# Kernel optimization log

Measured on AMD Instinct MI355X. Metric: run time of the kernel, lower is better.

The kernel has to match this reference:

```python
import jax, jax.numpy as jnp
import numpy as np

M, N, D, P, N_kv = 512, 4096, 128, 3584, 1024
H, H_kv = N // D, N_kv // D          # 32 query heads, 8 kv heads
G = H // H_kv                        # group size 4
L = P + M                            # cache length 4096


def setup_inputs() -> dict:
    key = jax.random.key(0)
    ks = jax.random.split(key, 6)
    w_scale = 0.008  # ~0.5/sqrt(N): keeps unscaled exp-softmax logits in fp32 range
    return {
        "X": jax.random.normal(ks[0], (M, N), jnp.float32),
        "W_q": jax.random.normal(ks[1], (N, N), jnp.float32) * w_scale,
        "W_k": jax.random.normal(ks[2], (N, N_kv), jnp.float32) * w_scale,
        "W_v": jax.random.normal(ks[3], (N, N_kv), jnp.float32) * w_scale,
        "cache_K": jax.random.normal(ks[4], (H, L, D), jnp.float32) * 0.02,
        "cache_V": jax.random.normal(ks[5], (H, L, D), jnp.float32) * 0.02,
    }


def reference(X, W_q, W_k, W_v, cache_K, cache_V):
    # fused QKV projection
    W_qkv = jnp.concatenate([W_q, W_k, W_v], axis=1)        # [N, N + 2*N_kv]
    qkv = X @ W_qkv                                          # [M, N + 2*N_kv]
    q = qkv[:, :N].reshape(M, H, D).transpose(1, 0, 2)       # [H, M, D]
    k = qkv[:, N:N + N_kv].reshape(M, H_kv, D).transpose(1, 0, 2)   # [H_kv, M, D]
    v = qkv[:, N + N_kv:].reshape(M, H_kv, D).transpose(1, 0, 2)    # [H_kv, M, D]
    # expand grouped KV heads (repeat_interleave) and append to cache at P
    k_exp = jnp.repeat(k, G, axis=0)                         # [H, M, D]
    v_exp = jnp.repeat(v, G, axis=0)
    Kc = cache_K.at[:, P:P + M, :].set(k_exp)                # [H, L, D]
    Vc = cache_V.at[:, P:P + M, :].set(v_exp)
    # naive (unscaled, non-max-subtracted) softmax attention over full cache
    scores = jnp.einsum('hmd,hld->hml', q, Kc)               # [H, M, L]
    e = jnp.exp(scores)
    weights = e / jnp.sum(e, axis=-1, keepdims=True)
    out = jnp.einsum('hml,hld->hmd', weights, Vc)            # [H, M, D]
    return out.transpose(1, 0, 2).reshape(M, H * D)          # [M, N]
```

## Files before the change

### kernel.cpp

```cpp
#include <hip/hip_runtime.h>
#include <hip/hip_bf16.h>

typedef __attribute__((ext_vector_type(8))) short short8;
typedef __attribute__((ext_vector_type(4))) float f32x4;

#define M_   512
#define N_   4096
#define D_   128
#define P_   3584
#define NKV  1024
#define L_   4096
#define H_   32
#define LOG2E 1.44269504088896340736f

__device__ __forceinline__ ushort f2bf(float f) {
  union { float f; unsigned u; } v; v.f = f;
  unsigned r = (v.u + 0x7fffu + ((v.u >> 16) & 1u)) >> 16;
  return (ushort)r;
}
__device__ __forceinline__ float bf2f(ushort u) {
  union { unsigned u; float f; } v; v.u = ((unsigned)u) << 16;
  return v.f;
}
__device__ __forceinline__ float fexp2(float x) {
  return __builtin_amdgcn_exp2f(x);
}
__device__ __forceinline__ unsigned pk2bf(float a, float b) {
  union { __hip_bfloat162 h; unsigned u; } cv;
  cv.h = __float22bfloat162_rn(make_float2(a, b));
  return cv.u;
}

__device__ __forceinline__ void gload_lds16(const void* g, void* l) {
  __builtin_amdgcn_global_load_lds(
      (const __attribute__((address_space(1))) void*)g,
      (__attribute__((address_space(3))) void*)l, 16, 0, 0);
}

__global__ __launch_bounds__(256) void xconv(const float* __restrict__ X,
                                             ushort* __restrict__ Xs)
{
  int g = blockIdx.x * 256 + threadIdx.x;
  int row = g >> 9;
  int cir = g & 511;
  int grp = cir >> 3, ch = cir & 7;
  const float* src = &X[(size_t)row * 4096 + cir * 8];
  float4 f0 = *reinterpret_cast<const float4*>(src);
  float4 f1 = *reinterpret_cast<const float4*>(src + 4);
  short8 s;
  s[0] = f2bf(f0.x); s[1] = f2bf(f0.y); s[2] = f2bf(f0.z); s[3] = f2bf(f0.w);
  s[4] = f2bf(f1.x); s[5] = f2bf(f1.y); s[6] = f2bf(f1.z); s[7] = f2bf(f1.w);
  int dcol = grp * 64 + ((ch ^ (row & 7)) * 8);
  *reinterpret_cast<short8*>(&Xs[(size_t)row * 4096 + dcol]) = s;
}

__global__ __launch_bounds__(256) void wtrans(
    const float* __restrict__ Wq, const float* __restrict__ Wk,
    const float* __restrict__ Wv, ushort* __restrict__ Wt)
{
  int bx = blockIdx.x;
  int by = blockIdx.y;
  const float* W; int wcols, c0;
  if (by < 64)      { W = Wq; wcols = 4096; c0 = by * 64; }
  else if (by < 80) { W = Wk; wcols = 1024; c0 = (by - 64) * 64; }
  else              { W = Wv; wcols = 1024; c0 = (by - 80) * 64; }
  int orow0 = by * 64;
  int r0 = bx * 64;
  __shared__ float T[64][65];
  int tid = threadIdx.x;

  #pragma unroll
  for (int i = 0; i < 4; ++i) {
    int r = i * 16 + (tid >> 4);
    int c4 = tid & 15;
    float4 f = *reinterpret_cast<const float4*>(&W[(size_t)(r0 + r) * wcols + c0 + c4 * 4]);
    T[r][c4 * 4 + 0] = f.x; T[r][c4 * 4 + 1] = f.y;
    T[r][c4 * 4 + 2] = f.z; T[r][c4 * 4 + 3] = f.w;
  }
  __syncthreads();

  #pragma unroll
  for (int i = 0; i < 2; ++i) {
    int j = i * 256 + tid;
    int orr = j >> 3;
    int ch = j & 7;
    short8 s;
    #pragma unroll
    for (int e = 0; e < 8; ++e) s[e] = f2bf(T[ch * 8 + e][orr]);
    int orow = orow0 + orr;
    int dstch = ch ^ (orow & 7);
    *reinterpret_cast<short8*>(&Wt[(size_t)orow * 4096 + r0 + dstch * 8]) = s;
  }
}

#define GEMM_STAGE(buf, k0g) do {                                             \
    _Pragma("unroll")                                                         \
    for (int i_ = 0; i_ < 4; ++i_) {                                          \
      int blk_ = w * 4 + i_;                                                  \
      gload_lds16(Asrc + (size_t)(blk_ * 8 + (lane >> 3)) * 4096 + (k0g) + (lane & 7) * 8, \
                  &As[buf][blk_ * 512]);                                      \
    }                                                                         \
    _Pragma("unroll")                                                         \
    for (int i_ = 0; i_ < 4; ++i_) {                                          \
      int blk_ = w * 4 + i_;                                                  \
      gload_lds16(Bsrc + (size_t)(blk_ * 8 + (lane >> 3)) * 4096 + (k0g) + (lane & 7) * 8, \
                  &Bs[buf][blk_ * 512]);                                      \
    }                                                                         \
  } while (0)

__global__ __launch_bounds__(256, 2) void qkv_gemm3(
    const ushort* __restrict__ Xs, const ushort* __restrict__ Wt,
    float* __restrict__ pg)
{
  const int bx = blockIdx.x;
  const int by = blockIdx.y;
  const int bz = blockIdx.z;
  const int tid = threadIdx.x, lane = tid & 63, w = tid >> 6;
  const int wr = w >> 1, wc = w & 1;
  const int m0 = by * 128, n0 = bx * 128;
  const int kb0 = bz * 2048;

  __shared__ ushort As[2][128 * 64];
  __shared__ ushort Bs[2][128 * 64];

  f32x4 acc[4][4];
  #pragma unroll
  for (int m = 0; m < 4; ++m)
    #pragma unroll
    for (int n = 0; n < 4; ++n)
      acc[m][n] = (f32x4){0.f, 0.f, 0.f, 0.f};

  const ushort* Asrc = Xs + (size_t)m0 * 4096;
  const ushort* Bsrc = Wt + (size_t)n0 * 4096;

  GEMM_STAGE(0, kb0);
  __syncthreads();
  int cur = 0;

  for (int kt = 0; kt < 32; ++kt) {
    if (kt + 1 < 32) GEMM_STAGE(cur ^ 1, kb0 + (kt + 1) * 64);
    #pragma unroll
    for (int kk = 0; kk < 2; ++kk) {
      short8 a[4], b[4];
      #pragma unroll
      for (int m = 0; m < 4; ++m) {
        int row = wr * 64 + m * 16 + (lane & 15);
        int ch = (kk * 4 + (lane >> 4)) ^ (row & 7);
        a[m] = *reinterpret_cast<const short8*>(&As[cur][row * 64 + ch * 8]);
      }
      #pragma unroll
      for (int n = 0; n < 4; ++n) {
        int row = wc * 64 + n * 16 + (lane & 15);
        int ch = (kk * 4 + (lane >> 4)) ^ (row & 7);
        b[n] = *reinterpret_cast<const short8*>(&Bs[cur][row * 64 + ch * 8]);
      }
      #pragma unroll
      for (int m = 0; m < 4; ++m)
        #pragma unroll
        for (int n = 0; n < 4; ++n)
          acc[m][n] = __builtin_amdgcn_mfma_f32_16x16x32_bf16(a[m], b[n], acc[m][n], 0, 0, 0);
    }
    __syncthreads();
    cur ^= 1;
  }

  float* dst = pg + (size_t)bz * 512 * 6144;
  #pragma unroll
  for (int m = 0; m < 4; ++m)
    #pragma unroll
    for (int n = 0; n < 4; ++n)
      #pragma unroll
      for (int j = 0; j < 4; ++j) {
        int row = m0 + wr * 64 + m * 16 + (lane >> 4) * 4 + j;
        int col = n0 + wc * 64 + n * 16 + (lane & 15);
        dst[(size_t)row * 6144 + col] = acc[m][n][j];
      }
}

__global__ __launch_bounds__(256) void combine_qk(
    const float* __restrict__ pg, ushort* __restrict__ qb,
    ushort* __restrict__ Kbn)
{
  int id = blockIdx.x * 256 + threadIdx.x;
  int m = id / 640;
  int c8 = (id - m * 640) * 8;
  const float* p0 = pg + (size_t)m * 6144 + c8;
  const float* p1 = p0 + (size_t)512 * 6144;
  if (c8 < 4096) {
    short8 s;
    #pragma unroll
    for (int e = 0; e < 8; ++e) s[e] = f2bf((p0[e] + p1[e]) * LOG2E);
    *reinterpret_cast<short8*>(&qb[(size_t)m * 4096 + c8]) = s;
  } else {
    short8 s;
    #pragma unroll
    for (int e = 0; e < 8; ++e) s[e] = f2bf(p0[e] + p1[e]);
    int o = c8 - 4096;
    int hk = o >> 7, d0 = o & 127;
    #pragma unroll
    for (int g = 0; g < 4; ++g)
      *reinterpret_cast<short8*>(&Kbn[((size_t)(hk * 4 + g) * 512 + m) * 128 + d0]) = s;
  }
}

__global__ __launch_bounds__(256) void combine_v(
    const float* __restrict__ pg, ushort* __restrict__ Vtn)
{
  int bz = blockIdx.x;
  int mt = bz & 7, hk = (bz >> 3) & 7, dh = bz >> 6;
  int m0 = mt * 64;
  int d0 = dh * 64;
  int colbase = 5120 + hk * 128 + d0;
  __shared__ float T[64][65];
  int tid = threadIdx.x;
  int r = tid >> 2, q4 = tid & 3;

  #pragma unroll
  for (int i = 0; i < 4; ++i) {
    int c = (q4 * 4 + i) * 4;
    const float* p0 = pg + (size_t)(m0 + r) * 6144 + colbase + c;
    const float* p1 = p0 + (size_t)512 * 6144;
    float4 a = *reinterpret_cast<const float4*>(p0);
    float4 b = *reinterpret_cast<const float4*>(p1);
    T[r][c + 0] = a.x + b.x; T[r][c + 1] = a.y + b.y;
    T[r][c + 2] = a.z + b.z; T[r][c + 3] = a.w + b.w;
  }
  __syncthreads();

  #pragma unroll
  for (int p = 0; p < 2; ++p) {
    int idx = p * 256 + tid;
    int dloc = idx >> 3, cc = idx & 7;
    int half = cc >> 2, c4 = (cc & 3) * 4;
    short8 s;
    #pragma unroll
    for (int e = 0; e < 8; ++e) {
      int lrow = half * 32 + c4 + (e < 4 ? e : 16 + (e - 4));
      s[e] = f2bf(T[lrow][dloc]);
    }
    int d = d0 + dloc;
    #pragma unroll
    for (int g = 0; g < 4; ++g) {
      int h = hk * 4 + g;
      *reinterpret_cast<short8*>(&Vtn[((size_t)h * 128 + d) * (size_t)L_ + P_ + m0 + cc * 8]) = s;
    }
  }
}

__global__ __launch_bounds__(256) void vconv(
    const float* __restrict__ cacheV, ushort* __restrict__ Vtn)
{
  int h = blockIdx.x, lt = blockIdx.y, dh = blockIdx.z;
  int l0 = lt * 64, d0 = dh * 64;
  __shared__ float T[64][65];
  int tid = threadIdx.x;
  int r4 = tid >> 4, c = tid & 15;

  #pragma unroll
  for (int p = 0; p < 4; ++p) {
    int r = p * 16 + r4;
    float4 f = *reinterpret_cast<const float4*>(
        &cacheV[((size_t)h * L_ + l0 + r) * 128 + d0 + c * 4]);
    T[r][c * 4 + 0] = f.x; T[r][c * 4 + 1] = f.y;
    T[r][c * 4 + 2] = f.z; T[r][c * 4 + 3] = f.w;
  }
  __syncthreads();

  int dr = tid >> 2, part = tid & 3;
  int d = d0 + dr;
  #pragma unroll
  for (int q = 0; q < 2; ++q) {
    int cc = part * 2 + q;
    int half = cc >> 2, c4 = (cc & 3) * 4;
    short8 s;
    #pragma unroll
    for (int e = 0; e < 8; ++e) {
      int lrow = half * 32 + c4 + (e < 4 ? e : 16 + (e - 4));
      s[e] = f2bf(T[lrow][dr]);
    }
    *reinterpret_cast<short8*>(&Vtn[((size_t)h * 128 + d) * (size_t)L_ + l0 + cc * 8]) = s;
  }
}

#define ATTN_TILE(bufc) do {                                                  \
    const ushort* Ksb = &Ks[bufc][0];                                         \
    const ushort* Vsb = &Vt[bufc][0];                                         \
    f32x4 sc0 = (f32x4){0.f, 0.f, 0.f, 0.f};                                  \
    f32x4 sc1 = (f32x4){0.f, 0.f, 0.f, 0.f};                                  \
    __builtin_amdgcn_s_setprio(1);                                            \
    _Pragma("unroll")                                                         \
    for (int kk = 0; kk < 4; ++kk) {                                          \
      int ch = (kk * 4 + hi) ^ (lo16 & 7);                                    \
      short8 a0 = *reinterpret_cast<const short8*>(&Ksb[lo16 * 128 + ch * 8]); \
      short8 a1 = *reinterpret_cast<const short8*>(&Ksb[(16 + lo16) * 128 + ch * 8]); \
      sc0 = __builtin_amdgcn_mfma_f32_16x16x32_bf16(a0, qreg[kk], sc0, 0, 0, 0); \
      sc1 = __builtin_amdgcn_mfma_f32_16x16x32_bf16(a1, qreg[kk], sc1, 0, 0, 0); \
    }                                                                         \
    __builtin_amdgcn_s_setprio(0);                                            \
    short8 pa;                                                                \
    {                                                                         \
      float e0 = fexp2(sc0[0]); float e1 = fexp2(sc0[1]);                     \
      float e2 = fexp2(sc0[2]); float e3 = fexp2(sc0[3]);                     \
      float f0 = fexp2(sc1[0]); float f1 = fexp2(sc1[1]);                     \
      float f2 = fexp2(sc1[2]); float f3 = fexp2(sc1[3]);                     \
      rs += ((e0 + e1) + (e2 + e3)) + ((f0 + f1) + (f2 + f3));                \
      union { unsigned u[4]; short8 s; } pk_;                                 \
      pk_.u[0] = pk2bf(e0, e1); pk_.u[1] = pk2bf(e2, e3);                     \
      pk_.u[2] = pk2bf(f0, f1); pk_.u[3] = pk2bf(f2, f3);                     \
      pa = pk_.s;                                                             \
    }                                                                         \
    __builtin_amdgcn_s_setprio(1);                                            \
    _Pragma("unroll")                                                         \
    for (int n = 0; n < 8; ++n) {                                             \
      int d = n * 16 + lo16;                                                  \
      int chv = hi ^ ((d >> 1) & 3);                                          \
      short8 bn = *reinterpret_cast<const short8*>(&Vsb[d * 32 + chv * 8]);   \
      o[n] = __builtin_amdgcn_mfma_f32_16x16x32_bf16(pa, bn, o[n], 0, 0, 0);  \
    }                                                                         \
    __builtin_amdgcn_s_setprio(0);                                            \
  } while (0)

#define AISSUE(t_) do {                                                       \
    if (s3 && (t_) >= 16) {                                                   \
      krn = *reinterpret_cast<const short8*>(                                 \
          &KsrcN[(size_t)((t_) * 32 - 512 + klr) * 128 + kc * 8]);            \
    } else {                                                                  \
      const float* kp_ = &Ksrc[(size_t)((t_) * 32 + klr) * 128 + kc * 8];     \
      kr0 = *reinterpret_cast<const float4*>(kp_);                            \
      kr1 = *reinterpret_cast<const float4*>(kp_ + 4);                        \
    }                                                                         \
    vrn = *reinterpret_cast<const short8*>(                                   \
        &VsrcN[(size_t)vd * (size_t)L_ + (t_) * 32 + vc3 * 8]);               \
  } while (0)

#define AWRITE(t_) do {                                                       \
    short8 ks_;                                                               \
    if (s3 && (t_) >= 16) { ks_ = krn; }                                      \
    else {                                                                    \
      union { unsigned u[4]; short8 s; } kk_;                                 \
      kk_.u[0] = pk2bf(kr0.x, kr0.y); kk_.u[1] = pk2bf(kr0.z, kr0.w);         \
      kk_.u[2] = pk2bf(kr1.x, kr1.y); kk_.u[3] = pk2bf(kr1.z, kr1.w);         \
      ks_ = kk_.s;                                                            \
    }                                                                         \
    *reinterpret_cast<short8*>(&Ks[(t_) & 3][klr * 128 + ((kc ^ (klr & 7)) * 8)]) = ks_; \
    *reinterpret_cast<short8*>(&Vt[(t_) & 3][vd * 32 + (((vc3 ^ (vd >> 1)) & 3) * 8)]) = vrn; \
  } while (0)

__global__ __launch_bounds__(512, 4) void gqa_attn15(
    const ushort* __restrict__ qb, const float* __restrict__ cacheK,
    const ushort* __restrict__ Kbn, const ushort* __restrict__ Vtn,
    ushort* __restrict__ pob, float* __restrict__ prs)
{
  const int b = blockIdx.x;
  const int s = b & 3;
  const int j = b >> 2;
  const int qt = j & 3;
  const int h = j >> 2;
  const int tid = threadIdx.x, lane = tid & 63, w = tid >> 6;
  const int lo16 = lane & 15, hi = lane >> 4;

  __shared__ ushort Ks[4][32 * 128];
  __shared__ ushort Vt[4][128 * 32];

  short8 qreg[4];
  {
    int qrow = qt * 128 + w * 16 + lo16;
    #pragma unroll
    for (int kk = 0; kk < 4; ++kk)
      qreg[kk] = *reinterpret_cast<const short8*>(
          &qb[(size_t)qrow * 4096 + h * 128 + (kk * 4 + hi) * 8]);
  }

  f32x4 o[8];
  #pragma unroll
  for (int n = 0; n < 8; ++n)
    o[n] = (f32x4){0.f, 0.f, 0.f, 0.f};
  float rs = 0.f;

  const int klr = tid >> 4, kc = tid & 15;
  const int vd = tid >> 2, vc3 = tid & 3;
  const float* Ksrc = cacheK + ((size_t)h * L_ + s * 1024) * 128;
  const ushort* KsrcN = Kbn + (size_t)h * 512 * 128;
  const ushort* VsrcN = Vtn + (size_t)h * 128 * (size_t)L_ + s * 1024;
  const bool s3 = (s == 3);

  float4 kr0, kr1;
  short8 krn, vrn;

  AISSUE(0);
  AWRITE(0);
  AISSUE(1);
  asm volatile("s_waitcnt lgkmcnt(0)" ::: "memory");
  __builtin_amdgcn_s_barrier();

  for (int t = 0; t < 32; ++t) {
    if (t + 1 < 32) AWRITE(t + 1);
    if (t + 2 < 32) AISSUE(t + 2);
    ATTN_TILE(t & 3);
    asm volatile("s_waitcnt lgkmcnt(0)" ::: "memory");
    __builtin_amdgcn_s_barrier();
  }

  float rsum = rs;
  rsum += __shfl_xor(rsum, 16, 64);
  rsum += __shfl_xor(rsum, 32, 64);

  const size_t pbase = (size_t)(s * 32 + h) * 512;
  #pragma unroll
  for (int n = 0; n < 8; ++n)
    #pragma unroll
    for (int j2 = 0; j2 < 4; ++j2) {
      int row = qt * 128 + w * 16 + hi * 4 + j2;
      pob[(pbase + row) * 128 + n * 16 + lo16] = f2bf(o[n][j2]);
    }
  if (hi == 0) {
    int row = qt * 128 + w * 16 + lo16;
    prs[pbase + row] = rsum;
  }
}

__global__ __launch_bounds__(256) void reduce_out(
    const ushort* __restrict__ pob, const float* __restrict__ prs,
    float* __restrict__ out)
{
  int id = blockIdx.x * 256 + threadIdx.x;
  int m = id >> 10, dq = id & 1023;
  int h = dq >> 5, d4 = dq & 31;
  float4 acc = {0.f, 0.f, 0.f, 0.f};
  float rsum = 0.f;
  #pragma unroll
  for (int s = 0; s < 4; ++s) {
    size_t base = (size_t)(s * 32 + h) * 512 + m;
    ushort4 v = *reinterpret_cast<const ushort4*>(&pob[base * 128 + d4 * 4]);
    acc.x += bf2f(v.x); acc.y += bf2f(v.y); acc.z += bf2f(v.z); acc.w += bf2f(v.w);
    rsum += prs[base];
  }
  float inv = 1.f / rsum;
  float4 r; r.x = acc.x * inv; r.y = acc.y * inv; r.z = acc.z * inv; r.w = acc.w * inv;
  *reinterpret_cast<float4*>(&out[(size_t)m * 4096 + dq * 4]) = r;
}

extern "C" void kernel_launch(void* const* d_in, const int* in_sizes, int n_in,
                              void* d_out, int out_size, void* d_ws, size_t ws_size,
                              hipStream_t stream) {
  const float* X  = (const float*)d_in[0];
  const float* Wq = (const float*)d_in[1];
  const float* Wk = (const float*)d_in[2];
  const float* Wv = (const float*)d_in[3];
  const float* cK = (const float*)d_in[4];
  const float* cV = (const float*)d_in[5];
  float* out = (float*)d_out;

  ushort* qb  = (ushort*)d_ws;
  ushort* Xs  = qb  + (size_t)M_ * N_;
  ushort* Kbn = Xs  + (size_t)M_ * N_;
  ushort* Vtn = Kbn + (size_t)H_ * 512 * D_;
  float*  prs = (float*)(Vtn + (size_t)H_ * D_ * L_);
  ushort* pob = (ushort*)(prs + 8 * 32 * 512);
  ushort* Wt  = pob + (size_t)4 * H_ * 512 * D_;
  float*  pg  = (float*)(Wt + (size_t)6144 * 4096);

  xconv<<<1024, 256, 0, stream>>>(X, Xs);
  wtrans<<<dim3(64, 96), 256, 0, stream>>>(Wq, Wk, Wv, Wt);
  qkv_gemm3<<<dim3(48, 4, 2), 256, 0, stream>>>(Xs, Wt, pg);
  combine_qk<<<1280, 256, 0, stream>>>(pg, qb, Kbn);
  combine_v<<<128, 256, 0, stream>>>(pg, Vtn);
  vconv<<<dim3(32, 56, 2), 256, 0, stream>>>(cV, Vtn);
  gqa_attn15<<<512, 512, 0, stream>>>(qb, cK, Kbn, Vtn, pob, prs);
  reduce_out<<<2048, 256, 0, stream>>>(pob, prs, out);
}
```

Measured before the change: 161.8 us.

## Process two 16-row query fragments per wave to double K/V tile reuse

Each wave in the attention kernel now computes two 16-row query fragments against every K/V tile staged in shared memory, so each block covers 256 query rows and the grid halves. This halves the global K/V loads and fp32-to-bf16 conversions per query row, and doubles the MFMA work per LDS read. In exchange, accumulator and query registers double, the occupancy hint drops, and fewer blocks are available to fill the GPU.

```diff
diff --git a/kernel.cpp b/kernel.cpp
--- a/kernel.cpp
+++ b/kernel.cpp
@@ -285,29 +285,37 @@
 #define ATTN_TILE(bufc) do {                                                  \
     const ushort* Ksb = &Ks[bufc][0];                                         \
     const ushort* Vsb = &Vt[bufc][0];                                         \
-    f32x4 sc0 = (f32x4){0.f, 0.f, 0.f, 0.f};                                  \
-    f32x4 sc1 = (f32x4){0.f, 0.f, 0.f, 0.f};                                  \
+    f32x4 sc[2][2];                                                           \
+    _Pragma("unroll")                                                         \
+    for (int f = 0; f < 2; ++f)                                               \
+      _Pragma("unroll")                                                       \
+      for (int mb = 0; mb < 2; ++mb)                                          \
+        sc[f][mb] = (f32x4){0.f, 0.f, 0.f, 0.f};                              \
     __builtin_amdgcn_s_setprio(1);                                            \
     _Pragma("unroll")                                                         \
     for (int kk = 0; kk < 4; ++kk) {                                          \
       int ch = (kk * 4 + hi) ^ (lo16 & 7);                                    \
       short8 a0 = *reinterpret_cast<const short8*>(&Ksb[lo16 * 128 + ch * 8]); \
       short8 a1 = *reinterpret_cast<const short8*>(&Ksb[(16 + lo16) * 128 + ch * 8]); \
-      sc0 = __builtin_amdgcn_mfma_f32_16x16x32_bf16(a0, qreg[kk], sc0, 0, 0, 0); \
-      sc1 = __builtin_amdgcn_mfma_f32_16x16x32_bf16(a1, qreg[kk], sc1, 0, 0, 0); \
+      _Pragma("unroll")                                                       \
+      for (int f = 0; f < 2; ++f) {                                           \
+        sc[f][0] = __builtin_amdgcn_mfma_f32_16x16x32_bf16(a0, qreg[f][kk], sc[f][0], 0, 0, 0); \
+        sc[f][1] = __builtin_amdgcn_mfma_f32_16x16x32_bf16(a1, qreg[f][kk], sc[f][1], 0, 0, 0); \
+      }                                                                       \
     }                                                                         \
     __builtin_amdgcn_s_setprio(0);                                            \
-    short8 pa;                                                                \
-    {                                                                         \
-      float e0 = fexp2(sc0[0]); float e1 = fexp2(sc0[1]);                     \
-      float e2 = fexp2(sc0[2]); float e3 = fexp2(sc0[3]);                     \
-      float f0 = fexp2(sc1[0]); float f1 = fexp2(sc1[1]);                     \
-      float f2 = fexp2(sc1[2]); float f3 = fexp2(sc1[3]);                     \
-      rs += ((e0 + e1) + (e2 + e3)) + ((f0 + f1) + (f2 + f3));                \
+    short8 pa[2];                                                             \
+    _Pragma("unroll")                                                         \
+    for (int f = 0; f < 2; ++f) {                                             \
+      float e0 = fexp2(sc[f][0][0]); float e1 = fexp2(sc[f][0][1]);           \
+      float e2 = fexp2(sc[f][0][2]); float e3 = fexp2(sc[f][0][3]);           \
+      float g0 = fexp2(sc[f][1][0]); float g1 = fexp2(sc[f][1][1]);           \
+      float g2 = fexp2(sc[f][1][2]); float g3 = fexp2(sc[f][1][3]);           \
+      rs[f] += ((e0 + e1) + (e2 + e3)) + ((g0 + g1) + (g2 + g3));             \
       union { unsigned u[4]; short8 s; } pk_;                                 \
       pk_.u[0] = pk2bf(e0, e1); pk_.u[1] = pk2bf(e2, e3);                     \
-      pk_.u[2] = pk2bf(f0, f1); pk_.u[3] = pk2bf(f2, f3);                     \
-      pa = pk_.s;                                                             \
+      pk_.u[2] = pk2bf(g0, g1); pk_.u[3] = pk2bf(g2, g3);                     \
+      pa[f] = pk_.s;                                                          \
     }                                                                         \
     __builtin_amdgcn_s_setprio(1);                                            \
     _Pragma("unroll")                                                         \
@@ -315,7 +323,8 @@
       int d = n * 16 + lo16;                                                  \
       int chv = hi ^ ((d >> 1) & 3);                                          \
       short8 bn = *reinterpret_cast<const short8*>(&Vsb[d * 32 + chv * 8]);   \
-      o[n] = __builtin_amdgcn_mfma_f32_16x16x32_bf16(pa, bn, o[n], 0, 0, 0);  \
+      o[0][n] = __builtin_amdgcn_mfma_f32_16x16x32_bf16(pa[0], bn, o[0][n], 0, 0, 0); \
+      o[1][n] = __builtin_amdgcn_mfma_f32_16x16x32_bf16(pa[1], bn, o[1][n], 0, 0, 0); \
     }                                                                         \
     __builtin_amdgcn_s_setprio(0);                                            \
   } while (0)
@@ -346,7 +355,7 @@
     *reinterpret_cast<short8*>(&Vt[(t_) & 3][vd * 32 + (((vc3 ^ (vd >> 1)) & 3) * 8)]) = vrn; \
   } while (0)
 
-__global__ __launch_bounds__(512, 4) void gqa_attn15(
+__global__ __launch_bounds__(512, 2) void gqa_attn16(
     const ushort* __restrict__ qb, const float* __restrict__ cacheK,
     const ushort* __restrict__ Kbn, const ushort* __restrict__ Vtn,
     ushort* __restrict__ pob, float* __restrict__ prs)
@@ -354,28 +363,31 @@
   const int b = blockIdx.x;
   const int s = b & 3;
   const int j = b >> 2;
-  const int qt = j & 3;
-  const int h = j >> 2;
+  const int qt = j & 1;
+  const int h = j >> 1;
   const int tid = threadIdx.x, lane = tid & 63, w = tid >> 6;
   const int lo16 = lane & 15, hi = lane >> 4;
 
   __shared__ ushort Ks[4][32 * 128];
   __shared__ ushort Vt[4][128 * 32];
 
-  short8 qreg[4];
-  {
-    int qrow = qt * 128 + w * 16 + lo16;
+  short8 qreg[2][4];
+  #pragma unroll
+  for (int f = 0; f < 2; ++f) {
+    int qrow = qt * 256 + w * 32 + f * 16 + lo16;
     #pragma unroll
     for (int kk = 0; kk < 4; ++kk)
-      qreg[kk] = *reinterpret_cast<const short8*>(
+      qreg[f][kk] = *reinterpret_cast<const short8*>(
           &qb[(size_t)qrow * 4096 + h * 128 + (kk * 4 + hi) * 8]);
   }
 
-  f32x4 o[8];
-  #pragma unroll
-  for (int n = 0; n < 8; ++n)
-    o[n] = (f32x4){0.f, 0.f, 0.f, 0.f};
-  float rs = 0.f;
+  f32x4 o[2][8];
+  #pragma unroll
+  for (int f = 0; f < 2; ++f)
+    #pragma unroll
+    for (int n = 0; n < 8; ++n)
+      o[f][n] = (f32x4){0.f, 0.f, 0.f, 0.f};
+  float rs[2] = {0.f, 0.f};
 
   const int klr = tid >> 4, kc = tid & 15;
   const int vd = tid >> 2, vc3 = tid & 3;
@@ -401,21 +413,31 @@
     __builtin_amdgcn_s_barrier();
   }
 
-  float rsum = rs;
-  rsum += __shfl_xor(rsum, 16, 64);
-  rsum += __shfl_xor(rsum, 32, 64);
+  float rsum[2];
+  #pragma unroll
+  for (int f = 0; f < 2; ++f) {
+    float v = rs[f];
+    v += __shfl_xor(v, 16, 64);
+    v += __shfl_xor(v, 32, 64);
+    rsum[f] = v;
+  }
 
   const size_t pbase = (size_t)(s * 32 + h) * 512;
   #pragma unroll
-  for (int n = 0; n < 8; ++n)
-    #pragma unroll
-    for (int j2 = 0; j2 < 4; ++j2) {
-      int row = qt * 128 + w * 16 + hi * 4 + j2;
-      pob[(pbase + row) * 128 + n * 16 + lo16] = f2bf(o[n][j2]);
+  for (int f = 0; f < 2; ++f)
+    #pragma unroll
+    for (int n = 0; n < 8; ++n)
+      #pragma unroll
+      for (int j2 = 0; j2 < 4; ++j2) {
+        int row = qt * 256 + w * 32 + f * 16 + hi * 4 + j2;
+        pob[(pbase + row) * 128 + n * 16 + lo16] = f2bf(o[f][n][j2]);
+      }
+  if (hi == 0) {
+    #pragma unroll
+    for (int f = 0; f < 2; ++f) {
+      int row = qt * 256 + w * 32 + f * 16 + lo16;
+      prs[pbase + row] = rsum[f];
     }
-  if (hi == 0) {
-    int row = qt * 128 + w * 16 + lo16;
-    prs[pbase + row] = rsum;
   }
 }
 
@@ -466,6 +488,6 @@
   combine_qk<<<1280, 256, 0, stream>>>(pg, qb, Kbn);
   combine_v<<<128, 256, 0, stream>>>(pg, Vtn);
   vconv<<<dim3(32, 56, 2), 256, 0, stream>>>(cV, Vtn);
-  gqa_attn15<<<512, 512, 0, stream>>>(qb, cK, Kbn, Vtn, pob, prs);
+  gqa_attn16<<<256, 512, 0, stream>>>(qb, cK, Kbn, Vtn, pob, prs);
   reduce_out<<<2048, 256, 0, stream>>>(pob, prs, out);
 }
```

Measured after the change: 168.3 us. +4.0%, slower.
